# Kernel optimization log

Measured on AMD Instinct MI355X. Metric: run time of the kernel, lower is better.

Reference implementation:

```python
import jax, jax.numpy as jnp
import numpy as np

T = 37          # bio_type_num
LP = T + 2      # padded label size (start, end)
START, END = T, T + 1


def crf_loglik(logits, labels, lens, trans):
    # logits: [B,S,LP] padded scores; labels: [B,S] ints; lens: [B]; trans[to, from]: [LP,LP]
    B, S, Lp = logits.shape
    dt = logits.dtype
    tpos = jnp.arange(S)
    mask = (tpos[None, :] < lens[:, None]).astype(dt)  # [B,S]
    # unary gold score
    unary = jnp.take_along_axis(logits, labels[..., None], axis=2)[..., 0] * mask
    # binary (transition) gold score with start/end extension
    labels_ext = jnp.concatenate([
        jnp.full((B, 1), START, labels.dtype), labels, jnp.full((B, 1), END, labels.dtype)], axis=1)  # [B,S+2]
    pos = jnp.arange(S + 2)
    labels_ext = jnp.where(pos[None, :] < (lens + 1)[:, None], labels_ext, END)
    frm, to = labels_ext[:, :-1], labels_ext[:, 1:]          # [B,S+1]
    trn_scr = trans[to, frm]                                  # [B,S+1]
    m2 = (jnp.arange(S + 1)[None, :] < (lens + 1)[:, None]).astype(dt)
    gold = unary.sum(1) + (trn_scr * m2).sum(1)               # [B]
    # partition function: forward algorithm (sequential scan over time)
    alpha0 = jnp.full((B, Lp), -100.0, dt).at[:, START].set(0.0)
    def step(alpha, xt):
        logit_t, m_t = xt                                     # [B,Lp], [B] bool
        mat = logit_t[:, :, None] + alpha[:, None, :] + trans[None, :, :]  # [B,to,from]
        alpha_nxt = jax.nn.logsumexp(mat, axis=2)
        alpha = jnp.where(m_t[:, None], alpha_nxt, alpha)
        return alpha, None
    xs = (jnp.swapaxes(logits, 0, 1), (tpos[None, :] < lens[:, None]).T)
    alpha, _ = jax.lax.scan(step, alpha0, xs)
    alpha = alpha + trans[END][None, :]
    norm = jax.nn.logsumexp(alpha, axis=1)                    # [B]
    return gold - norm


def ner_forward(h, bio_embed, W_cat, b_cat, W_crf, b_crf, transition, token_nums, entity_seq_labels):
    B, S, H = h.shape
    scale = 1.0 / jnp.sqrt(jnp.asarray(H, h.dtype))
    # one-head attention: query=token states, key=value=bio type embeddings (mask all ones -> no-op)
    scores = jnp.einsum('bsh,th->bst', h, bio_embed) * scale  # [B,S,T]
    attn = jax.nn.softmax(scores, axis=-1)
    aware = jnp.einsum('bst,th->bsh', attn, bio_embed)        # [B,S,H]
    x = jnp.concatenate([h, aware, h * aware], axis=-1)       # [B,S,3H]
    x = jax.nn.gelu(x @ W_cat + b_cat, approximate=False)     # [B,S,H]
    logits = x @ W_crf + b_crf                                # [B,S,T]
    pads = jnp.full((B, S, 2), -10000.0, logits.dtype)
    ner_scores = jnp.concatenate([logits, pads], axis=-1)     # [B,S,LP]
    ner_loss = crf_loglik(ner_scores, entity_seq_labels, token_nums, transition)
    return ner_scores, ner_loss


def setup_inputs() -> dict:
    key = jax.random.key(0)
    ks = jax.random.split(key, 8)
    B, S, H = 32, 512, 1024
    token_hidden_states = jax.random.normal(ks[0], (B, S, H), jnp.float32)
    token_masks = jnp.ones((B, S), jnp.bool_)
    token_nums = jax.random.randint(ks[1], (B,), 256, S + 1).at[0].set(S)
    entity_seq_labels = jax.random.randint(ks[2], (B, S), 0, T)
    bio_embed = jax.random.normal(ks[3], (T, H), jnp.float32) * 0.02
    W_cat = jax.random.normal(ks[4], (3 * H, H), jnp.float32) * (3.0 * H) ** -0.5
    b_cat = jnp.zeros((H,), jnp.float32)
    W_crf = jax.random.normal(ks[5], (H, T), jnp.float32) * H ** -0.5
    b_crf = jnp.zeros((T,), jnp.float32)
    transition = jax.random.normal(ks[6], (LP, LP), jnp.float32)
    return {
        'token_hidden_states': token_hidden_states, 'token_masks': token_masks,
        'token_nums': token_nums, 'entity_seq_labels': entity_seq_labels,
        'bio_embed': bio_embed, 'W_cat': W_cat, 'b_cat': b_cat,
        'W_crf': W_crf, 'b_crf': b_crf, 'transition': transition,
    }


def reference(token_hidden_states, token_masks, token_nums, entity_seq_labels,
              bio_embed, W_cat, b_cat, W_crf, b_crf, transition):
    # token_masks only generates an all-ones bio mask in the original (no-op); dropout in eval mode.
    return ner_forward(token_hidden_states, bio_embed, W_cat, b_cat, W_crf, b_crf,
                       transition, token_nums, entity_seq_labels)
```

## Files before the change

### kernel.cpp

```cpp
#include <hip/hip_runtime.h>
#include <hip/hip_bf16.h>
#include <math.h>

#define NB 32
#define NS 512
#define NH 1024
#define NT 37
#define NLP 39
#define NM (NB*NS)

typedef __attribute__((ext_vector_type(8))) short bf16x8;
typedef __attribute__((ext_vector_type(4))) float f32x4;

__device__ __forceinline__ float bf2f(unsigned int u) {
    unsigned int x = u << 16;
    float f;
    __builtin_memcpy(&f, &x, 4);
    return f;
}
__device__ __forceinline__ unsigned short f2bf(float f) {
    __hip_bfloat16 hb = __float2bfloat16(f);
    unsigned short u;
    __builtin_memcpy(&u, &hb, 2);
    return u;
}
__device__ __forceinline__ unsigned int pk2(float lo, float hi) {
    return ((unsigned int)f2bf(hi) << 16) | (unsigned int)f2bf(lo);
}
__device__ __forceinline__ int SW64(int b)  { return b ^ ((b >> 2) & 0x70); }
__device__ __forceinline__ int TSW(int row, int kcolByte) {
    return (row * 128 + kcolByte) ^ ((row & 7) << 4);
}
__device__ __forceinline__ float rl(float x, int l) {
    return __int_as_float(__builtin_amdgcn_readlane(__float_as_int(x), l));
}
__device__ __forceinline__ void gld16(const void* g, void* l) {
    __builtin_amdgcn_global_load_lds((const __attribute__((address_space(1))) void*)g,
                                     (__attribute__((address_space(3))) void*)l, 16, 0, 0);
}
#define VMW(N) asm volatile("s_waitcnt vmcnt(" #N ")" ::: "memory")
#define BARR() do { __builtin_amdgcn_s_barrier(); __builtin_amdgcn_sched_barrier(0); } while (0)

__global__ __launch_bounds__(256) void kPre(const float* __restrict__ h,
                                            const float* __restrict__ bio,
                                            const float* __restrict__ Wcat,
                                            const float* __restrict__ Wcrf,
                                            unsigned short* __restrict__ attn,
                                            char* __restrict__ Asw,
                                            char* __restrict__ Wsw,
                                            unsigned short* __restrict__ WT) {
    __shared__ __align__(16) char shmem[48 * 2048];
    const int bid = blockIdx.x;
    const int tid = threadIdx.x;

    if (bid < 256) {
        char* Bl = shmem;
        const int lane = tid & 63;
        const int wid  = tid >> 6;
        const int lr   = lane & 15;
        const int lk   = lane >> 4;
        const int m0   = bid * 64;
        const int tm   = bid >> 1;
        const int rbase = (bid & 1) * 64 + wid * 16 + lr;

        for (int idx = tid; idx < 37 * 256; idx += 256) {
            int t = idx >> 8, k4 = idx & 255;
            float4 v = *(const float4*)&bio[(size_t)t * NH + k4 * 4];
            int byte = (t * 2048 + k4 * 8) ^ ((t & 7) << 4);
            *(uint2*)(Bl + byte) = make_uint2(pk2(v.x, v.y), pk2(v.z, v.w));
        }
        for (int idx = tid; idx < 11 * 256; idx += 256) {
            int t = 37 + (idx >> 8), k4 = idx & 255;
            int byte = (t * 2048 + k4 * 8) ^ ((t & 7) << 4);
            *(uint2*)(Bl + byte) = make_uint2(0, 0);
        }
        __syncthreads();

        const int arow = m0 + wid * 16 + lr;
        const float* hp = h + (size_t)arow * NH + lk * 8;

        f32x4 sacc[3];
#pragma unroll
        for (int j = 0; j < 3; ++j) sacc[j] = (f32x4){0.f, 0.f, 0.f, 0.f};

        float4 p0 = *(const float4*)(hp);
        float4 p1 = *(const float4*)(hp + 4);
        for (int kt = 0; kt < NH; kt += 32) {
            float4 c0 = p0, c1 = p1;
            if (kt + 32 < NH) {
                p0 = *(const float4*)(hp + kt + 32);
                p1 = *(const float4*)(hp + kt + 36);
            }
            union { unsigned int u[4]; bf16x8 v; uint4 q; } af;
            af.u[0] = pk2(c0.x, c0.y); af.u[1] = pk2(c0.z, c0.w);
            af.u[2] = pk2(c1.x, c1.y); af.u[3] = pk2(c1.z, c1.w);
            {
                int kg = kt + lk * 8;
                size_t tb = ((size_t)tm * 48 + (kg >> 6)) * 16384;
                *(uint4*)(Asw + tb + TSW(rbase, (kg & 63) * 2)) = af.q;
            }
#pragma unroll
            for (int nf = 0; nf < 3; ++nf) {
                int t = nf * 16 + lr;
                int byte = (t * 2048 + (kt + lk * 8) * 2) ^ ((t & 7) << 4);
                bf16x8 bf = *(const bf16x8*)(Bl + byte);
                sacc[nf] = __builtin_amdgcn_mfma_f32_16x16x32_bf16(af.v, bf, sacc[nf], 0, 0, 0);
            }
        }

#pragma unroll
        for (int r = 0; r < 4; ++r) {
            const int orow = wid * 16 + lk * 4 + r;
            float s0 = sacc[0][r] * 0.03125f;
            float s1 = sacc[1][r] * 0.03125f;
            float s2 = sacc[2][r] * 0.03125f;
            const bool v2 = (lr < 5);
            float mx = fmaxf(fmaxf(s0, s1), v2 ? s2 : -1e30f);
#pragma unroll
            for (int d = 1; d < 16; d <<= 1) mx = fmaxf(mx, __shfl_xor(mx, d, 64));
            float e0 = __expf(s0 - mx), e1 = __expf(s1 - mx);
            float e2 = v2 ? __expf(s2 - mx) : 0.f;
            float sm = e0 + e1 + e2;
#pragma unroll
            for (int d = 1; d < 16; d <<= 1) sm += __shfl_xor(sm, d, 64);
            float inv = 1.f / sm;
            size_t g = (size_t)(m0 + orow) * 64;
            attn[g + lr]      = f2bf(e0 * inv);
            attn[g + 16 + lr] = f2bf(e1 * inv);
            attn[g + 32 + lr] = f2bf(e2 * inv);
            attn[g + 48 + lr] = 0;
        }
    } else if (bid < 640) {
        unsigned short* wt = (unsigned short*)shmem;
        const int tile = bid - 256;
        const int tn   = tile / 48;
        const int tk   = tile - tn * 48;
        const int n00  = tn * 128;
        const int k0   = tk * 64;

        for (int lin = tid; lin < 2048; lin += 256) {
            int kk = lin >> 5, ng = lin & 31;
            float4 v = *(const float4*)&Wcat[(size_t)(k0 + kk) * NH + n00 + ng * 4];
            *(uint2*)&wt[kk * 128 + ng * 4] = make_uint2(pk2(v.x, v.y), pk2(v.z, v.w));
        }
        __syncthreads();
        for (int lin = tid; lin < 1024; lin += 256) {
            int rn = lin >> 3, kg = lin & 7;
            unsigned short t8[8];
#pragma unroll
            for (int j = 0; j < 8; ++j) t8[j] = wt[(kg * 8 + j) * 128 + rn];
            uint4 v;
            __builtin_memcpy(&v, t8, 16);
            *(uint4*)(Wsw + (size_t)tile * 16384 + TSW(rn, kg * 16)) = v;
        }
    } else {
        const int idx = (bid - 640) * 256 + tid;
        if (idx < 48 * 384) {
            const int t = idx / 384, kg = idx - t * 384;
            unsigned short v[8];
#pragma unroll
            for (int e = 0; e < 8; ++e) {
                int k = kg * 8 + e;
                v[e] = (t < NT) ? f2bf(Wcrf[(size_t)k * NT + t]) : (unsigned short)0;
            }
            uint4 w;
            __builtin_memcpy(&w, v, 16);
            *(uint4*)(WT + (size_t)t * 3072 + kg * 8) = w;
        }
    }
}

__global__ __launch_bounds__(512) void kA1(const float* __restrict__ h,
                                           const float* __restrict__ bio,
                                           unsigned short* __restrict__ attn) {
    __shared__ __align__(16) char Bl[48 * 2048];

    const int tid  = threadIdx.x;
    const int lane = tid & 63;
    const int wid  = tid >> 6;
    const int lr   = lane & 15;
    const int lk   = lane >> 4;
    const int m0   = blockIdx.x * 128;

    for (int idx = tid; idx < 37 * 256; idx += 512) {
        int t = idx >> 8, k4 = idx & 255;
        float4 v = *(const float4*)&bio[(size_t)t * NH + k4 * 4];
        int byte = (t * 2048 + k4 * 8) ^ ((t & 7) << 4);
        *(uint2*)(Bl + byte) = make_uint2(pk2(v.x, v.y), pk2(v.z, v.w));
    }
    for (int idx = tid; idx < 11 * 256; idx += 512) {
        int t = 37 + (idx >> 8), k4 = idx & 255;
        int byte = (t * 2048 + k4 * 8) ^ ((t & 7) << 4);
        *(uint2*)(Bl + byte) = make_uint2(0, 0);
    }
    __syncthreads();

    const int arow = m0 + wid * 16 + lr;
    const float* hp = h + (size_t)arow * NH + lk * 8;

    f32x4 sacc[3];
#pragma unroll
    for (int j = 0; j < 3; ++j) sacc[j] = (f32x4){0.f, 0.f, 0.f, 0.f};

    float4 p0 = *(const float4*)(hp);
    float4 p1 = *(const float4*)(hp + 4);
    for (int kt = 0; kt < NH; kt += 32) {
        float4 c0 = p0, c1 = p1;
        if (kt + 32 < NH) {
            p0 = *(const float4*)(hp + kt + 32);
            p1 = *(const float4*)(hp + kt + 36);
        }
        union { unsigned int u[4]; bf16x8 v; } af;
        af.u[0] = pk2(c0.x, c0.y); af.u[1] = pk2(c0.z, c0.w);
        af.u[2] = pk2(c1.x, c1.y); af.u[3] = pk2(c1.z, c1.w);
#pragma unroll
        for (int nf = 0; nf < 3; ++nf) {
            int t = nf * 16 + lr;
            int byte = (t * 2048 + (kt + lk * 8) * 2) ^ ((t & 7) << 4);
            bf16x8 bf = *(const bf16x8*)(Bl + byte);
            sacc[nf] = __builtin_amdgcn_mfma_f32_16x16x32_bf16(af.v, bf, sacc[nf], 0, 0, 0);
        }
    }

#pragma unroll
    for (int r = 0; r < 4; ++r) {
        const int orow = wid * 16 + lk * 4 + r;
        float s0 = sacc[0][r] * 0.03125f;
        float s1 = sacc[1][r] * 0.03125f;
        float s2 = sacc[2][r] * 0.03125f;
        const bool v2 = (lr < 5);
        float mx = fmaxf(fmaxf(s0, s1), v2 ? s2 : -1e30f);
#pragma unroll
        for (int d = 1; d < 16; d <<= 1) mx = fmaxf(mx, __shfl_xor(mx, d, 64));
        float e0 = __expf(s0 - mx), e1 = __expf(s1 - mx);
        float e2 = v2 ? __expf(s2 - mx) : 0.f;
        float sm = e0 + e1 + e2;
#pragma unroll
        for (int d = 1; d < 16; d <<= 1) sm += __shfl_xor(sm, d, 64);
        float inv = 1.f / sm;
        size_t g = (size_t)(m0 + orow) * 64;
        attn[g + lr]      = f2bf(e0 * inv);
        attn[g + 16 + lr] = f2bf(e1 * inv);
        attn[g + 32 + lr] = f2bf(e2 * inv);
        attn[g + 48 + lr] = 0;
    }
}

__global__ __launch_bounds__(256) void kA2(const unsigned short* __restrict__ attn,
                                           const float* __restrict__ bio,
                                           unsigned short* __restrict__ aware) {
    __shared__ __align__(16) char Bsl[128 * 64];

    const int tid  = threadIdx.x;
    const int lane = tid & 63;
    const int wid  = tid >> 6;
    const int wm   = (wid >> 1) * 64;
    const int wn   = (wid & 1) * 64;
    const int lr   = lane & 15;
    const int lk   = lane >> 4;
    const int n0   = blockIdx.x * 128;
    const int m0   = blockIdx.y * 128;

    const int bn = tid & 127;
    const int bq = (tid >> 7) * 16;

    f32x4 acc[4][4];
#pragma unroll
    for (int i = 0; i < 4; ++i)
#pragma unroll
        for (int j = 0; j < 4; ++j) acc[i][j] = (f32x4){0.f, 0.f, 0.f, 0.f};

#pragma unroll
    for (int ks = 0; ks < 2; ++ks) {
        unsigned int p[8];
#pragma unroll
        for (int i = 0; i < 8; ++i) {
            int t0 = ks*32 + bq + 2*i;
            float lo = (t0     < NT) ? bio[(size_t)t0 * NH + n0 + bn]       : 0.f;
            float hi = (t0 + 1 < NT) ? bio[(size_t)(t0+1) * NH + n0 + bn]   : 0.f;
            p[i] = pk2(lo, hi);
        }
        __syncthreads();
        *(int4*)(Bsl + SW64(bn*64 + bq*2))      = make_int4(p[0], p[1], p[2], p[3]);
        *(int4*)(Bsl + SW64(bn*64 + bq*2 + 16)) = make_int4(p[4], p[5], p[6], p[7]);
        __syncthreads();

        bf16x8 af[4];
#pragma unroll
        for (int mf = 0; mf < 4; ++mf)
            af[mf] = *(const bf16x8*)(attn + (size_t)(m0 + wm + mf*16 + lr) * 64 + ks*32 + lk*8);
#pragma unroll
        for (int nf = 0; nf < 4; ++nf) {
            bf16x8 bb = *(const bf16x8*)(Bsl + SW64((wn + nf*16 + lr)*64 + lk*16));
#pragma unroll
            for (int mf = 0; mf < 4; ++mf)
                acc[mf][nf] = __builtin_amdgcn_mfma_f32_16x16x32_bf16(af[mf], bb, acc[mf][nf], 0, 0, 0);
        }
    }

#pragma unroll
    for (int mf = 0; mf < 4; ++mf)
#pragma unroll
        for (int nf = 0; nf < 4; ++nf)
#pragma unroll
            for (int r = 0; r < 4; ++r) {
                size_t row = (size_t)(m0 + wm + mf*16 + lk*4 + r);
                aware[row * NH + n0 + wn + nf*16 + lr] = f2bf(acc[mf][nf][r]);
            }
}

__global__ __launch_bounds__(256) void kA2f(const unsigned short* __restrict__ attn,
                                            const float* __restrict__ bio,
                                            char* __restrict__ Asw) {
    __shared__ __align__(16) char Bsl[128 * 64];
    __shared__ __align__(16) unsigned short awL[128 * 128];

    const int tid  = threadIdx.x;
    const int lane = tid & 63;
    const int wid  = tid >> 6;
    const int wm   = (wid >> 1) * 64;
    const int wn   = (wid & 1) * 64;
    const int lr   = lane & 15;
    const int lk   = lane >> 4;
    const int n0   = blockIdx.x * 128;
    const int m0   = blockIdx.y * 128;
    const int tm   = blockIdx.y;

    const int bn = tid & 127;
    const int bq = (tid >> 7) * 16;

    f32x4 acc[4][4];
#pragma unroll
    for (int i = 0; i < 4; ++i)
#pragma unroll
        for (int j = 0; j < 4; ++j) acc[i][j] = (f32x4){0.f, 0.f, 0.f, 0.f};

#pragma unroll
    for (int ks = 0; ks < 2; ++ks) {
        unsigned int p[8];
#pragma unroll
        for (int i = 0; i < 8; ++i) {
            int t0 = ks*32 + bq + 2*i;
            float lo = (t0     < NT) ? bio[(size_t)t0 * NH + n0 + bn]       : 0.f;
            float hi = (t0 + 1 < NT) ? bio[(size_t)(t0+1) * NH + n0 + bn]   : 0.f;
            p[i] = pk2(lo, hi);
        }
        __syncthreads();
        *(int4*)(Bsl + SW64(bn*64 + bq*2))      = make_int4(p[0], p[1], p[2], p[3]);
        *(int4*)(Bsl + SW64(bn*64 + bq*2 + 16)) = make_int4(p[4], p[5], p[6], p[7]);
        __syncthreads();

        bf16x8 af[4];
#pragma unroll
        for (int mf = 0; mf < 4; ++mf)
            af[mf] = *(const bf16x8*)(attn + (size_t)(m0 + wm + mf*16 + lr) * 64 + ks*32 + lk*8);
#pragma unroll
        for (int nf = 0; nf < 4; ++nf) {
            bf16x8 bb = *(const bf16x8*)(Bsl + SW64((wn + nf*16 + lr)*64 + lk*16));
#pragma unroll
            for (int mf = 0; mf < 4; ++mf)
                acc[mf][nf] = __builtin_amdgcn_mfma_f32_16x16x32_bf16(af[mf], bb, acc[mf][nf], 0, 0, 0);
        }
    }

#pragma unroll
    for (int mf = 0; mf < 4; ++mf)
#pragma unroll
        for (int nf = 0; nf < 4; ++nf)
#pragma unroll
            for (int r = 0; r < 4; ++r)
                awL[(wm + mf*16 + lk*4 + r) * 128 + wn + nf*16 + lr] = f2bf(acc[mf][nf][r]);
    __syncthreads();

#pragma unroll
    for (int i = 0; i < 8; ++i) {
        int lin = tid + i * 256;
        int row = lin >> 4, kg = lin & 15;
        uint4 v = *(const uint4*)&awL[row * 128 + kg * 8];
        int kglob = 1024 + n0 + kg * 8;
        size_t tbase = ((size_t)tm * 48 + (kglob >> 6)) * 16384;
        *(uint4*)(Asw + tbase + TSW(row, (kglob & 63) * 2)) = v;
    }
#pragma unroll
    for (int i = 0; i < 8; ++i) {
        int lin = tid + i * 256;
        int row = lin >> 4, kg = lin & 15;
        int k0g = n0 + kg * 8;
        size_t tb0 = ((size_t)tm * 48 + (k0g >> 6)) * 16384;
        uint4 hv4 = *(const uint4*)(Asw + tb0 + TSW(row, (k0g & 63) * 2));
        unsigned int hu[4] = {hv4.x, hv4.y, hv4.z, hv4.w};
        uint4 awv = *(const uint4*)&awL[row * 128 + kg * 8];
        unsigned int awu[4] = {awv.x, awv.y, awv.z, awv.w};
        unsigned int p2[4];
#pragma unroll
        for (int j = 0; j < 4; ++j) {
            float lo = bf2f(hu[j] & 0xffffu) * bf2f(awu[j] & 0xffffu);
            float hi = bf2f(hu[j] >> 16)     * bf2f(awu[j] >> 16);
            p2[j] = pk2(lo, hi);
        }
        int k2g = 2048 + n0 + kg * 8;
        size_t tb2 = ((size_t)tm * 48 + (k2g >> 6)) * 16384;
        *(uint4*)(Asw + tb2 + TSW(row, (k2g & 63) * 2)) = make_uint4(p2[0], p2[1], p2[2], p2[3]);
    }
}

__global__ __launch_bounds__(512, 2) void kBf(const char* __restrict__ Asw,
                                              const char* __restrict__ Wsw,
                                              const float* __restrict__ bcat,
                                              const unsigned short* __restrict__ WT,
                                              float* __restrict__ P) {
    __shared__ __align__(16) char lds[131072];

    const int tid  = threadIdx.x;
    const int lane = tid & 63;
    const int wid  = tid >> 6;
    const int widm = wid >> 2;
    const int widn = wid & 3;
    const int lr   = lane & 15;
    const int lk   = lane >> 4;

    const int id   = blockIdx.x;
    const int xcd  = id & 7;
    const int slot = id >> 3;
    const int Mt   = xcd * 8 + (slot >> 2);
    const int Nt   = slot & 3;
    const int m0   = Mt * 256, n0 = Nt * 256;
    const int soff = tid * 16;

    f32x4 acc00[4][2], acc01[4][2], acc10[4][2], acc11[4][2];
#pragma unroll
    for (int i = 0; i < 4; ++i)
#pragma unroll
        for (int j = 0; j < 2; ++j) {
            acc00[i][j] = (f32x4){0.f,0.f,0.f,0.f};
            acc01[i][j] = (f32x4){0.f,0.f,0.f,0.f};
            acc10[i][j] = (f32x4){0.f,0.f,0.f,0.f};
            acc11[i][j] = (f32x4){0.f,0.f,0.f,0.f};
        }

    auto stageHalf = [&](int T, int ph) {
        const bool isA = (ph == 0) || (ph == 3);
        const int  h   = isA ? (ph == 3 ? 1 : 0) : (ph - 1);
        const char* src = isA
            ? Asw + ((size_t)((2*Mt + h) * 48 + T)) * 16384
            : Wsw + ((size_t)((2*Nt + h) * 48 + T)) * 16384;
        char* dst = lds + (isA ? 0 : 65536) + (T & 1) * 32768 + h * 16384;
        gld16(src + soff,        dst + soff);
        gld16(src + soff + 8192, dst + soff + 8192);
    };
    auto loadA = [&](bf16x8 (&af)[4][2], int q, int half) {
        const char* base = lds + q * 32768 + half * 16384;
#pragma unroll
        for (int i = 0; i < 4; ++i) {
            int row = widm * 64 + i * 16 + lr;
#pragma unroll
            for (int kk = 0; kk < 2; ++kk)
                af[i][kk] = *(const bf16x8*)(base + TSW(row, kk * 64 + lk * 16));
        }
    };
    auto loadB = [&](bf16x8 (&bfr)[2][2], int q, int half) {
        const char* base = lds + 65536 + q * 32768 + half * 16384;
#pragma unroll
        for (int j = 0; j < 2; ++j) {
            int col = widn * 32 + j * 16 + lr;
#pragma unroll
            for (int kk = 0; kk < 2; ++kk)
                bfr[j][kk] = *(const bf16x8*)(base + TSW(col, kk * 64 + lk * 16));
        }
    };
    auto mma = [&](f32x4 (&ac)[4][2], bf16x8 (&af)[4][2], bf16x8 (&bfr)[2][2]) {
        __builtin_amdgcn_s_setprio(1);
#pragma unroll
        for (int kk = 0; kk < 2; ++kk)
#pragma unroll
            for (int i = 0; i < 4; ++i)
#pragma unroll
                for (int j = 0; j < 2; ++j)
                    ac[i][j] = __builtin_amdgcn_mfma_f32_16x16x32_bf16(
                        af[i][kk], bfr[j][kk], ac[i][j], 0, 0, 0);
        __builtin_amdgcn_s_setprio(0);
    };

    stageHalf(0, 0); stageHalf(0, 1); stageHalf(0, 2); stageHalf(0, 3);
    VMW(0);
    BARR();

    for (int T = 0; T < 48; ++T) {
        const int q = T & 1;
        const bool pf = (T + 1 < 48);
        bf16x8 af0[4][2], af1[4][2], bf0[2][2], bf1[2][2];

        if (T > 0) {
            if (pf) { stageHalf(T + 1, 0); VMW(2); }
            else    { VMW(0); }
            BARR();
        } else if (pf) {
            stageHalf(T + 1, 0);
        }

        loadA(af0, q, 0); loadB(bf0, q, 0);
        if (pf) stageHalf(T + 1, 1);
        BARR();
        mma(acc00, af0, bf0);

        loadB(bf1, q, 1);
        if (pf) stageHalf(T + 1, 2);
        BARR();
        mma(acc01, af0, bf1);

        loadA(af1, q, 1);
        if (pf) stageHalf(T + 1, 3);
        BARR();
        mma(acc10, af1, bf0);

        BARR();
        mma(acc11, af1, bf1);
    }

    __syncthreads();
    auto stashQ = [&](f32x4 (&ac)[4][2], int a, int b) {
#pragma unroll
        for (int j = 0; j < 2; ++j) {
            const int lcol = b * 128 + widn * 32 + j * 16 + lr;
            const int kc = lcol >> 6, kk = lcol & 63;
            const float bc = bcat[n0 + lcol];
#pragma unroll
            for (int i = 0; i < 4; ++i)
#pragma unroll
                for (int r = 0; r < 4; ++r) {
                    int lrow = a * 128 + widm * 64 + i * 16 + lk * 4 + r;
                    float x = ac[i][j][r] + bc;
                    float g = 0.5f * x * (1.0f + erff(x * 0.70710678118654752f));
                    *(unsigned short*)(lds + kc * 32768 + TSW(lrow, kk * 2)) = f2bf(g);
                }
        }
    };
    stashQ(acc00, 0, 0); stashQ(acc01, 0, 1); stashQ(acc10, 1, 0); stashQ(acc11, 1, 1);
    __syncthreads();

    bf16x8 wfrag[3][8];
#pragma unroll
    for (int tt = 0; tt < 3; ++tt) {
        const int t = tt * 16 + lr;
#pragma unroll
        for (int ks = 0; ks < 8; ++ks)
            wfrag[tt][ks] = *(const bf16x8*)(WT + (size_t)t * 3072 + n0 + ks * 32 + lk * 8);
    }

    f32x4 pacc[2][3];
#pragma unroll
    for (int i = 0; i < 2; ++i)
#pragma unroll
        for (int j = 0; j < 3; ++j) pacc[i][j] = (f32x4){0.f, 0.f, 0.f, 0.f};
#pragma unroll
    for (int rt2 = 0; rt2 < 2; ++rt2) {
        const int lrow = wid * 32 + rt2 * 16 + lr;
#pragma unroll
        for (int ks = 0; ks < 8; ++ks) {
            const int kc = ks >> 1, kh = ks & 1;
            bf16x8 af = *(const bf16x8*)(lds + kc * 32768 + TSW(lrow, kh * 64 + lk * 16));
#pragma unroll
            for (int tt = 0; tt < 3; ++tt)
                pacc[rt2][tt] = __builtin_amdgcn_mfma_f32_16x16x32_bf16(
                    af, wfrag[tt][ks], pacc[rt2][tt], 0, 0, 0);
        }
    }

    float* Pb = P + (size_t)Nt * NM * 48;
#pragma unroll
    for (int rt2 = 0; rt2 < 2; ++rt2)
#pragma unroll
        for (int tt = 0; tt < 3; ++tt)
#pragma unroll
            for (int r = 0; r < 4; ++r) {
                int row = Mt * 256 + wid * 32 + rt2 * 16 + lk * 4 + r;
                Pb[(size_t)row * 48 + tt * 16 + lr] = pacc[rt2][tt][r];
            }
}

__global__ __launch_bounds__(256) void kDmCr(const float* __restrict__ P,
                                             const float* __restrict__ bcrf,
                                             const int* __restrict__ lens,
                                             const float* __restrict__ trans,
                                             float* __restrict__ out,
                                             float* __restrict__ Pm,
                                             float* __restrict__ Pc) {
    __shared__ float el_all[64 * 64];
    __shared__ __align__(16) char Mb[2 * 6144];

    const int tid = threadIdx.x;
    const int b   = blockIdx.x >> 3;
    const int s   = blockIdx.x & 7;
    const int t0  = s * 64;
    const size_t STRIDE = (size_t)NM * 48;

    {
        const int i  = tid >> 2;
        const int tg = (tid & 3) * 12;
        const int gr = b * NS + t0 + i;
#pragma unroll
        for (int j = 0; j < 12; ++j) {
            int t = tg + j;
            size_t flat = (size_t)gr * 48 + t;
            float v = P[flat] + P[STRIDE + flat] + P[2*STRIDE + flat] + P[3*STRIDE + flat];
            float o, el;
            if (t < NT) { o = v + bcrf[t]; el = __expf(o); }
            else        { o = -10000.0f;   el = 0.f; }
            if (t < NLP) out[(size_t)gr * NLP + t] = o;
            el_all[i * 64 + t] = el;
        }
    }
    for (int z = tid; z < 64 * 16; z += 256)
        el_all[(z >> 4) * 64 + 48 + (z & 15)] = 0.f;
    __syncthreads();

    if (tid >= 64) return;

    const int lane = tid;
    const int lr   = lane & 15;
    const int lk   = lane >> 4;
    const int len  = lens[b];
    const int nsteps = (len > t0) ? ((len - t0 < 64) ? (len - t0) : 64) : 0;
    float* Pg = Pm + (size_t)(b * 8 + s) * 2304;

    if (nsteps == 0) {
        for (int j = 0; j < 36; ++j) Pg[j * 64 + lane] = 0.f;
        if (lane < 48) Pg[lane * 48 + lane] = 1.f;
        if (lane == 0) Pc[b * 8 + s] = 0.f;
        return;
    }

    bf16x8 Tf[3][2];
#pragma unroll
    for (int tt = 0; tt < 3; ++tt)
#pragma unroll
        for (int ks = 0; ks < 2; ++ks) {
            const int row = tt * 16 + lr;
            unsigned int u[4];
#pragma unroll
            for (int e2 = 0; e2 < 4; ++e2) {
                int f0 = ks * 32 + lk * 8 + 2 * e2;
                float lo = (row < NLP && f0     < NLP) ? __expf(trans[row * NLP + f0])     : 0.f;
                float hi = (row < NLP && f0 + 1 < NLP) ? __expf(trans[row * NLP + f0 + 1]) : 0.f;
                u[e2] = pk2(lo, hi);
            }
            union { unsigned int uu[4]; bf16x8 v; } cv;
            cv.uu[0]=u[0]; cv.uu[1]=u[1]; cv.uu[2]=u[2]; cv.uu[3]=u[3];
            Tf[tt][ks] = cv.v;
        }

    for (int j = 0; j < 48; ++j)
        *(unsigned int*)(Mb + j * 256 + lane * 4) = 0;
    if (lane < 48) {
        int byte = (lane * 128 + lane * 2) ^ ((lane & 7) << 4);
        *(unsigned short*)(Mb + byte) = f2bf(1.0f);
    }

    float Cacc = 0.f;

    for (int i = 0; i < nsteps; ++i) {
        const int q = i & 1;
        const char* Mr = Mb + q * 6144;

        bf16x8 Bf[3][2];
#pragma unroll
        for (int ct = 0; ct < 3; ++ct) {
#pragma unroll
            for (int ks = 0; ks < 2; ++ks) {
                int col = ct * 16 + lr;
                int byte = (col * 128 + (ks * 32 + lk * 8) * 2) ^ ((col & 7) << 4);
                Bf[ct][ks] = *(const bf16x8*)(Mr + byte);
            }
        }
        f32x4 el4[3];
#pragma unroll
        for (int tt = 0; tt < 3; ++tt)
            el4[tt] = *(const f32x4*)&el_all[i * 64 + tt * 16 + lk * 4];

        f32x4 c[3][3];
#pragma unroll
        for (int tt = 0; tt < 3; ++tt)
#pragma unroll
            for (int ct = 0; ct < 3; ++ct) {
                c[tt][ct] = __builtin_amdgcn_mfma_f32_16x16x32_bf16(
                    Tf[tt][0], Bf[ct][0], (f32x4){0.f,0.f,0.f,0.f}, 0, 0, 0);
                c[tt][ct] = __builtin_amdgcn_mfma_f32_16x16x32_bf16(
                    Tf[tt][1], Bf[ct][1], c[tt][ct], 0, 0, 0);
            }
#pragma unroll
        for (int tt = 0; tt < 3; ++tt)
#pragma unroll
            for (int ct = 0; ct < 3; ++ct)
#pragma unroll
                for (int r = 0; r < 4; ++r)
                    c[tt][ct][r] *= el4[tt][r];

        if ((i & 3) == 3) {
            float sv = rl(c[0][0][0], 0);
            float rr = __builtin_amdgcn_rcpf(sv);
#pragma unroll
            for (int tt = 0; tt < 3; ++tt)
#pragma unroll
                for (int ct = 0; ct < 3; ++ct)
#pragma unroll
                    for (int r = 0; r < 4; ++r) c[tt][ct][r] *= rr;
            Cacc -= __logf(rr);
        }

        if (i == nsteps - 1) {
#pragma unroll
            for (int tt = 0; tt < 3; ++tt)
#pragma unroll
                for (int ct = 0; ct < 3; ++ct)
#pragma unroll
                    for (int r = 0; r < 4; ++r) {
                        int row = tt * 16 + lk * 4 + r;
                        int col = ct * 16 + lr;
                        Pg[row * 48 + col] = c[tt][ct][r];
                    }
        } else {
            char* Mw = Mb + (q ^ 1) * 6144;
#pragma unroll
            for (int tt = 0; tt < 3; ++tt)
#pragma unroll
                for (int ct = 0; ct < 3; ++ct) {
                    int col = ct * 16 + lr;
                    int k   = tt * 16 + lk * 4;
                    int byte = (col * 128 + k * 2) ^ ((col & 7) << 4);
                    *(uint2*)(Mw + byte) = make_uint2(pk2(c[tt][ct][0], c[tt][ct][1]),
                                                      pk2(c[tt][ct][2], c[tt][ct][3]));
                }
        }
    }

    if (lane == 0) Pc[b * 8 + s] = Cacc;
}

__global__ __launch_bounds__(256) void kDc(const float* __restrict__ scores,
                                           const int* __restrict__ labels,
                                           const int* __restrict__ lens,
                                           const float* __restrict__ trans,
                                           const float* __restrict__ Pm,
                                           const float* __restrict__ Pc,
                                           float* __restrict__ loss) {
    __shared__ float trL[39 * 41];
    __shared__ float gred[4];

    const int b    = blockIdx.x;
    const int tid  = threadIdx.x;
    const int lane = tid & 63;
    const int wid  = tid >> 6;
    const int len  = lens[b];
    const float* sb = scores + (size_t)b * NS * NLP;

    for (int idx = tid; idx < 39 * 39; idx += 256) {
        int to = idx / 39, f = idx - to * 39;
        trL[to * 41 + f] = trans[idx];
    }
    __syncthreads();

    float g = 0.0f;
    for (int t = tid; t < len; t += 256) g += sb[(size_t)t * NLP + labels[b * NS + t]];
    for (int i = tid; i <= len; i += 256) {
        int frm = (i == 0) ? 37 : labels[b * NS + i - 1];
        int to  = (i == len) ? 38 : labels[b * NS + i];
        g += trL[to * 41 + frm];
    }
#pragma unroll
    for (int off = 32; off > 0; off >>= 1) g += __shfl_xor(g, off, 64);
    if (lane == 0) gred[wid] = g;
    __syncthreads();

    if (wid != 0) return;

    const float gold = (gred[0] + gred[1]) + (gred[2] + gred[3]);
    const bool act48 = (lane < 48);

    const float* P0 = Pm + (size_t)b * 8 * 2304;
    float v = act48 ? P0[lane * 48 + 37] : 0.f;
    float C = Pc[b * 8];

    for (int s = 1; s < 8; ++s) {
        float as_[40];
#pragma unroll
        for (int f = 0; f < 40; ++f) as_[f] = rl(v, f);
        __builtin_amdgcn_sched_barrier(0);
        const float* Ps = Pm + (size_t)(b * 8 + s) * 2304;
        float c = 0.f;
        if (act48) {
            const float4* rowp = (const float4*)(Ps + lane * 48);
#pragma unroll
            for (int q = 0; q < 10; ++q) {
                float4 rv = rowp[q];
                c = fmaf(rv.x, as_[q*4+0], c);
                c = fmaf(rv.y, as_[q*4+1], c);
                c = fmaf(rv.z, as_[q*4+2], c);
                c = fmaf(rv.w, as_[q*4+3], c);
            }
        }
        float sv = rl(c, 0);
        float rr = __builtin_amdgcn_rcpf(sv);
        v = c * rr;
        C -= __logf(rr);
        C += Pc[b * 8 + s];
    }

    const float trEnd = (lane < NLP) ? trL[38 * 41 + lane] : 0.f;
    float aend = (lane < NLP && v > 0.f) ? C + __logf(v) + trEnd : -1e30f;
    float mx = aend;
#pragma unroll
    for (int off = 32; off > 0; off >>= 1) mx = fmaxf(mx, __shfl_xor(mx, off, 64));
    float es = (lane < NLP) ? __expf(aend - mx) : 0.f;
#pragma unroll
    for (int off = 32; off > 0; off >>= 1) es += __shfl_xor(es, off, 64);
    float norm = mx + __logf(es);

    if (lane == 0) loss[b] = gold - norm;
}

__global__ __launch_bounds__(256) void kB(const float* __restrict__ h,
                                          const unsigned short* __restrict__ aware,
                                          const float* __restrict__ Wcat,
                                          const float* __restrict__ bcat,
                                          unsigned short* __restrict__ x2) {
    __shared__ __align__(16) char lds[16384];
    char* Asl = lds;
    char* Bsl = lds + 8192;

    const int tid  = threadIdx.x;
    const int lane = tid & 63;
    const int wid  = tid >> 6;
    const int wm   = (wid >> 1) * 64;
    const int wn   = (wid & 1) * 64;
    const int lr   = lane & 15;
    const int lk   = lane >> 4;

    const int id   = blockIdx.x;
    const int xcd  = id & 7;
    const int slot = id >> 3;
    const int m0   = (xcd * 16 + (slot >> 3)) * 128;
    const int n0   = (slot & 7) * 128;

    const int am = tid >> 1;
    const int ak = (tid & 1) * 16;
    const int bn = tid & 127;
    const int bk = (tid >> 7) * 16;

    f32x4 acc[4][4];
#pragma unroll
    for (int i = 0; i < 4; ++i)
#pragma unroll
        for (int j = 0; j < 4; ++j) acc[i][j] = (f32x4){0.f, 0.f, 0.f, 0.f};

    const float*          hrow = h     + (size_t)(m0 + am) * NH + ak;
    const unsigned short* arow = aware + (size_t)(m0 + am) * NH + ak;
    const float*          wcol = Wcat  + (size_t)bk * NH + n0 + bn;

    float hv[16];
    unsigned int aw[8];
    float wv[16];

    auto stage = [&](int kt) {
        const int region = kt >> 10;
        const int kb = kt & 1023;
        if (region != 1) {
            const float4* hp = (const float4*)(hrow + kb);
            float4 a = hp[0], b = hp[1], c = hp[2], d = hp[3];
            hv[0]=a.x; hv[1]=a.y; hv[2]=a.z; hv[3]=a.w;
            hv[4]=b.x; hv[5]=b.y; hv[6]=b.z; hv[7]=b.w;
            hv[8]=c.x; hv[9]=c.y; hv[10]=c.z; hv[11]=c.w;
            hv[12]=d.x; hv[13]=d.y; hv[14]=d.z; hv[15]=d.w;
        }
        if (region >= 1) {
            const uint4* ap = (const uint4*)(arow + kb);
            uint4 a0 = ap[0], a1 = ap[1];
            aw[0]=a0.x; aw[1]=a0.y; aw[2]=a0.z; aw[3]=a0.w;
            aw[4]=a1.x; aw[5]=a1.y; aw[6]=a1.z; aw[7]=a1.w;
        }
        {
            const float* wp = wcol + (size_t)kt * NH;
#pragma unroll
            for (int j = 0; j < 16; ++j) wv[j] = wp[(size_t)j * NH];
        }
    };

    auto writeStage = [&](int kt) {
        const int region = kt >> 10;
        unsigned int p[8];
        if (region == 0) {
#pragma unroll
            for (int i = 0; i < 8; ++i) p[i] = pk2(hv[2*i], hv[2*i+1]);
        } else if (region == 1) {
#pragma unroll
            for (int i = 0; i < 8; ++i) p[i] = aw[i];
        } else {
#pragma unroll
            for (int i = 0; i < 8; ++i) {
                float lo = hv[2*i]   * bf2f(aw[i] & 0xffffu);
                float hi = hv[2*i+1] * bf2f(aw[i] >> 16);
                p[i] = pk2(lo, hi);
            }
        }
        *(int4*)(Asl + SW64(am*64 + ak*2))      = make_int4(p[0], p[1], p[2], p[3]);
        *(int4*)(Asl + SW64(am*64 + ak*2 + 16)) = make_int4(p[4], p[5], p[6], p[7]);
        unsigned int q[8];
#pragma unroll
        for (int i = 0; i < 8; ++i) q[i] = pk2(wv[2*i], wv[2*i+1]);
        *(int4*)(Bsl + SW64(bn*64 + bk*2))      = make_int4(q[0], q[1], q[2], q[3]);
        *(int4*)(Bsl + SW64(bn*64 + bk*2 + 16)) = make_int4(q[4], q[5], q[6], q[7]);
    };

    stage(0);
    for (int kt = 0; kt < 3072; kt += 32) {
        __syncthreads();
        writeStage(kt);
        __syncthreads();
        if (kt + 32 < 3072) stage(kt + 32);

        bf16x8 af[4], bfr[4];
#pragma unroll
        for (int mf = 0; mf < 4; ++mf)
            af[mf] = *(const bf16x8*)(Asl + SW64((wm + mf*16 + lr)*64 + lk*16));
#pragma unroll
        for (int nf = 0; nf < 4; ++nf)
            bfr[nf] = *(const bf16x8*)(Bsl + SW64((wn + nf*16 + lr)*64 + lk*16));
#pragma unroll
        for (int mf = 0; mf < 4; ++mf)
#pragma unroll
            for (int nf = 0; nf < 4; ++nf)
                acc[mf][nf] = __builtin_amdgcn_mfma_f32_16x16x32_bf16(af[mf], bfr[nf], acc[mf][nf], 0, 0, 0);
    }

#pragma unroll
    for (int nf = 0; nf < 4; ++nf) {
        const int col = n0 + wn + nf*16 + lr;
        const float bc = bcat[col];
#pragma unroll
        for (int mf = 0; mf < 4; ++mf)
#pragma unroll
            for (int r = 0; r < 4; ++r) {
                size_t row = (size_t)(m0 + wm + mf*16 + lk*4 + r);
                float x = acc[mf][nf][r] + bc;
                float g = 0.5f * x * (1.0f + erff(x * 0.70710678118654752f));
                x2[row * NH + col] = f2bf(g);
            }
    }
}

__global__ __launch_bounds__(256) void kC(const unsigned short* __restrict__ x2,
                                          const float* __restrict__ Wcrf,
                                          const float* __restrict__ bcrf,
                                          float* __restrict__ out) {
    __shared__ __align__(16) char Asl[8192];
    __shared__ __align__(16) char Bsl[3072];

    const int tid  = threadIdx.x;
    const int lane = tid & 63;
    const int wid  = tid >> 6;
    const int lr   = lane & 15;
    const int lk   = lane >> 4;
    const int m0   = blockIdx.x * 128;
    const int am   = tid >> 1;
    const int ak   = (tid & 1) * 16;

    for (int i = tid; i < 192; i += 256) *(int4*)(Bsl + i*16) = make_int4(0, 0, 0, 0);

    f32x4 acc[2][3];
#pragma unroll
    for (int i = 0; i < 2; ++i)
#pragma unroll
        for (int j = 0; j < 3; ++j) acc[i][j] = (f32x4){0.f, 0.f, 0.f, 0.f};

    const unsigned short* xrow = x2 + (size_t)(m0 + am) * NH + ak;

    for (int kt = 0; kt < NH; kt += 32) {
        const uint4* xp = (const uint4*)(xrow + kt);
        uint4 x0 = xp[0], x1 = xp[1];
        float wv[5];
#pragma unroll
        for (int p = 0; p < 5; ++p) {
            int i = tid + p * 256;
            wv[p] = (i < 32*NT) ? Wcrf[(size_t)kt * NT + i] : 0.f;
        }
        __syncthreads();
        *(uint4*)(Asl + SW64(am*64 + ak*2))      = x0;
        *(uint4*)(Asl + SW64(am*64 + ak*2 + 16)) = x1;
#pragma unroll
        for (int p = 0; p < 5; ++p) {
            int i = tid + p * 256;
            if (i < 32*NT) {
                int kk = i / NT;
                int t  = i - kk * NT;
                *(unsigned short*)(Bsl + SW64(t*64 + kk*2)) = f2bf(wv[p]);
            }
        }
        __syncthreads();
        bf16x8 af[2], bfr[3];
#pragma unroll
        for (int mf = 0; mf < 2; ++mf)
            af[mf] = *(const bf16x8*)(Asl + SW64((wid*32 + mf*16 + lr)*64 + lk*16));
#pragma unroll
        for (int nf = 0; nf < 3; ++nf)
            bfr[nf] = *(const bf16x8*)(Bsl + SW64((nf*16 + lr)*64 + lk*16));
#pragma unroll
        for (int mf = 0; mf < 2; ++mf)
#pragma unroll
            for (int nf = 0; nf < 3; ++nf)
                acc[mf][nf] = __builtin_amdgcn_mfma_f32_16x16x32_bf16(af[mf], bfr[nf], acc[mf][nf], 0, 0, 0);
    }

#pragma unroll
    for (int nf = 0; nf < 3; ++nf) {
        const int t = nf*16 + lr;
        const float bc = (t < NT) ? bcrf[t] : 0.f;
#pragma unroll
        for (int mf = 0; mf < 2; ++mf)
#pragma unroll
            for (int r = 0; r < 4; ++r) {
                size_t row = (size_t)(m0 + wid*32 + mf*16 + lk*4 + r);
                if (t < NT)       out[row * NLP + t] = acc[mf][nf][r] + bc;
                else if (t < NLP) out[row * NLP + t] = -10000.0f;
            }
    }
}

#define CRFSTEP(EL) do {                                   \
    float as_[37];                                         \
    _Pragma("unroll")                                      \
    for (int f_ = 0; f_ < 37; ++f_) as_[f_] = rl(a, f_);   \
    __builtin_amdgcn_sched_barrier(0);                     \
    float c0 = 0.f, c1 = 0.f, c2 = 0.f, c3 = 0.f;          \
    _Pragma("unroll")                                      \
    for (int f_ = 0; f_ < 36; f_ += 4) {                   \
        c0 = fmaf(as_[f_    ], trow[f_    ], c0);          \
        c1 = fmaf(as_[f_ + 1], trow[f_ + 1], c1);          \
        c2 = fmaf(as_[f_ + 2], trow[f_ + 2], c2);          \
        c3 = fmaf(as_[f_ + 3], trow[f_ + 3], c3);          \
    }                                                      \
    c0 = fmaf(as_[36], trow[36], c0);                      \
    a = (EL) * ((c0 + c1) + (c2 + c3));                    \
} while (0)

__global__ __launch_bounds__(256) void kDold(const float* __restrict__ scores,
                                             const int* __restrict__ labels,
                                             const int* __restrict__ lens,
                                             const float* __restrict__ trans,
                                             float* __restrict__ loss) {
    __shared__ float S[NS * NLP];
    __shared__ float trL[39 * 41];
    __shared__ int   labL[NS];
    __shared__ float gred[4];

    const int b    = blockIdx.x;
    const int tid  = threadIdx.x;
    const int lane = tid & 63;
    const int wid  = tid >> 6;
    const int len  = lens[b];
    const float* sb = scores + (size_t)b * NS * NLP;

    {
        const int n4 = (len * NLP + 3) >> 2;
        const float4* src = (const float4*)sb;
        float4* dst = (float4*)S;
        for (int i = tid; i < n4; i += 256) dst[i] = src[i];
    }
    for (int i = tid; i < NS; i += 256) labL[i] = labels[b * NS + i];
    for (int idx = tid; idx < 39 * 39; idx += 256) {
        int to = idx / 39, f = idx - to * 39;
        trL[to * 41 + f] = trans[idx];
    }
    __syncthreads();

    float g = 0.0f;
    for (int t = tid; t < len; t += 256) g += S[t * NLP + labL[t]];
    for (int i = tid; i <= len; i += 256) {
        int frm = (i == 0) ? 37 : labL[i - 1];
        int to  = (i == len) ? 38 : labL[i];
        g += trL[to * 41 + frm];
    }
#pragma unroll
    for (int off = 32; off > 0; off >>= 1) g += __shfl_xor(g, off, 64);
    if (lane == 0) gred[wid] = g;
    __syncthreads();

    if (wid != 0) return;

    const float gold = (gred[0] + gred[1]) + (gred[2] + gred[3]);

    const int myrow = (lane < 39) ? lane : 0;
    float trow[39];
#pragma unroll
    for (int f = 0; f < 39; ++f) trow[f] = __expf(trL[myrow * 41 + f]);
    const float trEnd = (lane < 39) ? trL[38 * 41 + lane] : 0.f;
    const bool act = (lane < 39);

    float l0 = act ? S[lane] : -10000.f;
    float a = act ? __expf(l0) * trow[37] : 0.f;
    float C = 0.0f;

    auto ldrow = [&](int r) {
        r = (r < len) ? r : (len - 1);
        return S[act ? (r * NLP + lane) : 0];
    };
    float lg0 = ldrow(1), lg1 = ldrow(2), lg2 = ldrow(3), lg3 = ldrow(4);

    int t = 1;
    for (; t + 3 < len; t += 4) {
        float e0 = __expf(lg0), e1 = __expf(lg1), e2 = __expf(lg2), e3 = __expf(lg3);
        lg0 = ldrow(t + 4); lg1 = ldrow(t + 5); lg2 = ldrow(t + 6); lg3 = ldrow(t + 7);
        CRFSTEP(e0); CRFSTEP(e1); CRFSTEP(e2); CRFSTEP(e3);
        float s = rl(a, 0);
        float rr = __builtin_amdgcn_rcpf(s);
        a *= rr; C -= __logf(rr);
    }
    for (; t < len; ++t) {
        float el = __expf(ldrow(t));
        CRFSTEP(el);
    }

    float aend = (act && a > 0.f) ? C + __logf(a) + trEnd : -1e30f;
    float mx = aend;
#pragma unroll
    for (int off = 32; off > 0; off >>= 1) mx = fmaxf(mx, __shfl_xor(mx, off, 64));
    float es = act ? __expf(aend - mx) : 0.0f;
#pragma unroll
    for (int off = 32; off > 0; off >>= 1) es += __shfl_xor(es, off, 64);
    float norm = mx + __logf(es);

    if (lane == 0) loss[b] = gold - norm;
}

extern "C" void kernel_launch(void* const* d_in, const int* in_sizes, int n_in,
                              void* d_out, int out_size, void* d_ws, size_t ws_size,
                              hipStream_t stream) {
    const float* h        = (const float*)d_in[0];
    const int* token_nums = (const int*)d_in[2];
    const int* labels     = (const int*)d_in[3];
    const float* bio      = (const float*)d_in[4];
    const float* Wcat     = (const float*)d_in[5];
    const float* bcat     = (const float*)d_in[6];
    const float* Wcrf     = (const float*)d_in[7];
    const float* bcrf     = (const float*)d_in[8];
    const float* trans    = (const float*)d_in[9];

    float* out = (float*)d_out;
    unsigned short* attn  = (unsigned short*)d_out;

    const size_t ASW_BYTES = (size_t)128 * 48 * 16384;
    const size_t P_BYTES   = (size_t)4 * NM * 48 * 4;
    const size_t WSW_BYTES = (size_t)8 * 48 * 16384;
    const size_t WT_BYTES  = (size_t)48 * 3072 * 2;
    const size_t PM_BYTES  = (size_t)NB * 8 * 2304 * 4;
    const size_t PC_BYTES  = (size_t)NB * 8 * 4;
    const bool fast = ws_size >= ASW_BYTES + P_BYTES + WSW_BYTES + WT_BYTES + PM_BYTES + PC_BYTES;

    if (fast) {
        char*  Asw = (char*)d_ws;
        float* P   = (float*)((char*)d_ws + ASW_BYTES);
        char*  Wsw = (char*)d_ws + ASW_BYTES + P_BYTES;
        unsigned short* WT = (unsigned short*)((char*)d_ws + ASW_BYTES + P_BYTES + WSW_BYTES);
        float* Pm  = (float*)((char*)d_ws + ASW_BYTES + P_BYTES + WSW_BYTES + WT_BYTES);
        float* Pc  = Pm + (size_t)NB * 8 * 2304;

        hipLaunchKernelGGL(kPre, dim3(712), dim3(256), 0, stream,
                           h, bio, Wcat, Wcrf, attn, Asw, Wsw, WT);
        hipLaunchKernelGGL(kA2f, dim3(NH / 128, NM / 128), dim3(256), 0, stream,
                           attn, bio, Asw);
        hipLaunchKernelGGL(kBf, dim3(256), dim3(512), 0, stream, Asw, Wsw, bcat, WT, P);
        hipLaunchKernelGGL(kDmCr, dim3(NB * 8), dim3(256), 0, stream,
                           P, bcrf, token_nums, trans, out, Pm, Pc);
        hipLaunchKernelGGL(kDc, dim3(NB), dim3(256), 0, stream, out, labels, token_nums,
                           trans, Pm, Pc, out + (size_t)NM * NLP);
    } else {
        unsigned short* aware = (unsigned short*)d_ws;
        unsigned short* x2    = aware + (size_t)NM * NH;

        hipLaunchKernelGGL(kA1, dim3(NM / 128), dim3(512), 0, stream, h, bio, attn);
        hipLaunchKernelGGL(kA2, dim3(NH / 128, NM / 128), dim3(256), 0, stream, attn, bio, aware);
        hipLaunchKernelGGL(kB, dim3((NH / 128) * (NM / 128)), dim3(256), 0, stream,
                           h, aware, Wcat, bcat, x2);
        hipLaunchKernelGGL(kC, dim3(NM / 128), dim3(256), 0, stream, x2, Wcrf, bcrf, out);
        hipLaunchKernelGGL(kDold, dim3(NB), dim3(256), 0, stream, out, labels, token_nums,
                           trans, out + (size_t)NM * NLP);
    }
}
```

Measured before the change: 212.6 us.

## Split CRF scan into 16 segments and batch GEMM LDS loads before MFMAs

The CRF forward pass is split into 16 segments of 32 timesteps instead of 8 segments of 64. This doubles the number of blocks computing segment transfer matrices in parallel and halves each block's sequential chain. The cost is a longer serial combine in the final reduction and a larger workspace. Separately, the GEMM inner loop now issues all LDS fragment loads and prefetch staging up front, then runs all four MFMAs with a single barrier. This removes three barriers per k-step at the cost of more live fragment registers.

```diff
diff --git a/kernel.cpp b/kernel.cpp
--- a/kernel.cpp
+++ b/kernel.cpp
@@ -8,6 +8,8 @@
 #define NT 37
 #define NLP 39
 #define NM (NB*NS)
+#define NSEG 16
+#define SEGLEN 32
 
 typedef __attribute__((ext_vector_type(8))) short bf16x8;
 typedef __attribute__((ext_vector_type(4))) float f32x4;
@@ -500,21 +502,15 @@
 
         loadA(af0, q, 0); loadB(bf0, q, 0);
         if (pf) stageHalf(T + 1, 1);
+        loadB(bf1, q, 1); loadA(af1, q, 1);
+        if (pf) { stageHalf(T + 1, 2); stageHalf(T + 1, 3); }
+
+        mma(acc00, af0, bf0);
+        mma(acc01, af0, bf1);
+        mma(acc10, af1, bf0);
+        mma(acc11, af1, bf1);
+
         BARR();
-        mma(acc00, af0, bf0);
-
-        loadB(bf1, q, 1);
-        if (pf) stageHalf(T + 1, 2);
-        BARR();
-        mma(acc01, af0, bf1);
-
-        loadA(af1, q, 1);
-        if (pf) stageHalf(T + 1, 3);
-        BARR();
-        mma(acc10, af1, bf0);
-
-        BARR();
-        mma(acc11, af1, bf1);
     }
 
     __syncthreads();
@@ -585,21 +581,21 @@
                                              float* __restrict__ out,
                                              float* __restrict__ Pm,
                                              float* __restrict__ Pc) {
-    __shared__ float el_all[64 * 64];
+    __shared__ float el_all[SEGLEN * 64];
     __shared__ __align__(16) char Mb[2 * 6144];
 
     const int tid = threadIdx.x;
-    const int b   = blockIdx.x >> 3;
-    const int s   = blockIdx.x & 7;
-    const int t0  = s * 64;
+    const int b   = blockIdx.x >> 4;
+    const int s   = blockIdx.x & 15;
+    const int t0  = s * SEGLEN;
     const size_t STRIDE = (size_t)NM * 48;
 
     {
-        const int i  = tid >> 2;
-        const int tg = (tid & 3) * 12;
+        const int i  = tid >> 3;
+        const int tg = (tid & 7) * 6;
         const int gr = b * NS + t0 + i;
 #pragma unroll
-        for (int j = 0; j < 12; ++j) {
+        for (int j = 0; j < 6; ++j) {
             int t = tg + j;
             size_t flat = (size_t)gr * 48 + t;
             float v = P[flat] + P[STRIDE + flat] + P[2*STRIDE + flat] + P[3*STRIDE + flat];
@@ -610,7 +606,7 @@
             el_all[i * 64 + t] = el;
         }
     }
-    for (int z = tid; z < 64 * 16; z += 256)
+    for (int z = tid; z < SEGLEN * 16; z += 256)
         el_all[(z >> 4) * 64 + 48 + (z & 15)] = 0.f;
     __syncthreads();
 
@@ -620,13 +616,13 @@
     const int lr   = lane & 15;
     const int lk   = lane >> 4;
     const int len  = lens[b];
-    const int nsteps = (len > t0) ? ((len - t0 < 64) ? (len - t0) : 64) : 0;
-    float* Pg = Pm + (size_t)(b * 8 + s) * 2304;
+    const int nsteps = (len > t0) ? ((len - t0 < SEGLEN) ? (len - t0) : SEGLEN) : 0;
+    float* Pg = Pm + (size_t)(b * NSEG + s) * 2304;
 
     if (nsteps == 0) {
         for (int j = 0; j < 36; ++j) Pg[j * 64 + lane] = 0.f;
         if (lane < 48) Pg[lane * 48 + lane] = 1.f;
-        if (lane == 0) Pc[b * 8 + s] = 0.f;
+        if (lane == 0) Pc[b * NSEG + s] = 0.f;
         return;
     }
 
@@ -733,7 +729,7 @@
         }
     }
 
-    if (lane == 0) Pc[b * 8 + s] = Cacc;
+    if (lane == 0) Pc[b * NSEG + s] = Cacc;
 }
 
 __global__ __launch_bounds__(256) void kDc(const float* __restrict__ scores,
@@ -776,16 +772,16 @@
     const float gold = (gred[0] + gred[1]) + (gred[2] + gred[3]);
     const bool act48 = (lane < 48);
 
-    const float* P0 = Pm + (size_t)b * 8 * 2304;
+    const float* P0 = Pm + (size_t)b * NSEG * 2304;
     float v = act48 ? P0[lane * 48 + 37] : 0.f;
-    float C = Pc[b * 8];
-
-    for (int s = 1; s < 8; ++s) {
+    float C = Pc[b * NSEG];
+
+    for (int s = 1; s < NSEG; ++s) {
         float as_[40];
 #pragma unroll
         for (int f = 0; f < 40; ++f) as_[f] = rl(v, f);
         __builtin_amdgcn_sched_barrier(0);
-        const float* Ps = Pm + (size_t)(b * 8 + s) * 2304;
+        const float* Ps = Pm + (size_t)(b * NSEG + s) * 2304;
         float c = 0.f;
         if (act48) {
             const float4* rowp = (const float4*)(Ps + lane * 48);
@@ -802,7 +798,7 @@
         float rr = __builtin_amdgcn_rcpf(sv);
         v = c * rr;
         C -= __logf(rr);
-        C += Pc[b * 8 + s];
+        C += Pc[b * NSEG + s];
     }
 
     const float trEnd = (lane < NLP) ? trL[38 * 41 + lane] : 0.f;
@@ -1150,8 +1146,8 @@
     const size_t P_BYTES   = (size_t)4 * NM * 48 * 4;
     const size_t WSW_BYTES = (size_t)8 * 48 * 16384;
     const size_t WT_BYTES  = (size_t)48 * 3072 * 2;
-    const size_t PM_BYTES  = (size_t)NB * 8 * 2304 * 4;
-    const size_t PC_BYTES  = (size_t)NB * 8 * 4;
+    const size_t PM_BYTES  = (size_t)NB * NSEG * 2304 * 4;
+    const size_t PC_BYTES  = (size_t)NB * NSEG * 4;
     const bool fast = ws_size >= ASW_BYTES + P_BYTES + WSW_BYTES + WT_BYTES + PM_BYTES + PC_BYTES;
 
     if (fast) {
@@ -1160,14 +1156,14 @@
         char*  Wsw = (char*)d_ws + ASW_BYTES + P_BYTES;
         unsigned short* WT = (unsigned short*)((char*)d_ws + ASW_BYTES + P_BYTES + WSW_BYTES);
         float* Pm  = (float*)((char*)d_ws + ASW_BYTES + P_BYTES + WSW_BYTES + WT_BYTES);
-        float* Pc  = Pm + (size_t)NB * 8 * 2304;
+        float* Pc  = Pm + (size_t)NB * NSEG * 2304;
 
         hipLaunchKernelGGL(kPre, dim3(712), dim3(256), 0, stream,
                            h, bio, Wcat, Wcrf, attn, Asw, Wsw, WT);
         hipLaunchKernelGGL(kA2f, dim3(NH / 128, NM / 128), dim3(256), 0, stream,
                            attn, bio, Asw);
         hipLaunchKernelGGL(kBf, dim3(256), dim3(512), 0, stream, Asw, Wsw, bcat, WT, P);
-        hipLaunchKernelGGL(kDmCr, dim3(NB * 8), dim3(256), 0, stream,
+        hipLaunchKernelGGL(kDmCr, dim3(NB * NSEG), dim3(256), 0, stream,
                            P, bcrf, token_nums, trans, out, Pm, Pc);
         hipLaunchKernelGGL(kDc, dim3(NB), dim3(256), 0, stream, out, labels, token_nums,
                            trans, Pm, Pc, out + (size_t)NM * NLP);
```

New measurement: 198.7 us. 6.6% less time.
